# Kernel optimization log

Measured on AMD Instinct MI355X. Metric: run time of the kernel, lower is better.

Reference implementation:

```python
import jax, jax.numpy as jnp
import numpy as np

V_BOOK, V_AUTH, V_LANG, V_TAG = 10001, 5001, 28, 34253
D = 32  # EMBED_DIM
B, C, LH, LW = 4096, 100, 200, 50


def setup_inputs() -> dict:
    key = jax.random.key(0)
    ks = jax.random.split(key, 32)
    it = iter(ks)

    def emb(k, v):
        t = jax.random.normal(k, (v, D), jnp.float32) * 0.05
        return t.at[0].set(0.0)  # padding_idx=0

    def lin(k, i, o):
        k1, k2 = jax.random.split(k)
        lim = 1.0 / np.sqrt(i)
        return (jax.random.uniform(k1, (i, o), jnp.float32, -lim, lim),
                jax.random.uniform(k2, (o,), jnp.float32, -lim, lim))

    hist = jax.random.randint(next(it), (B, LH), 0, V_BOOK)
    wish = jax.random.randint(next(it), (B, LW), 0, V_BOOK)
    cand = jax.random.randint(next(it), (B, C), 0, V_BOOK)
    auth = jax.random.randint(next(it), (B, C), 0, V_AUTH)
    lang = jax.random.randint(next(it), (B, C), 0, V_LANG)
    tags = jax.random.randint(next(it), (B, C, 5), 0, V_TAG)
    dense = jax.random.normal(next(it), (B, C, 3), jnp.float32)

    E_hist = emb(next(it), V_BOOK)
    E_wish = emb(next(it), V_BOOK)
    E_cand = emb(next(it), V_BOOK)
    E_auth = emb(next(it), V_AUTH)
    E_lang = emb(next(it), V_LANG)
    E_tags = emb(next(it), V_TAG)

    Wb0, bb0 = lin(next(it), 3, 32)
    Wb1, bb1 = lin(next(it), 32, D)
    Wt0, bt0 = lin(next(it), 2 * D, 256)
    Wt1, bt1 = lin(next(it), 256, 128)
    Wt2, bt2 = lin(next(it), 128, 64)
    Wt3, bt3 = lin(next(it), 64, 1)

    return dict(hist=hist, wish=wish, cand=cand, auth=auth, lang=lang, tags=tags,
                dense=dense, E_hist=E_hist, E_wish=E_wish, E_cand=E_cand,
                E_auth=E_auth, E_lang=E_lang, E_tags=E_tags,
                Wb0=Wb0, bb0=bb0, Wb1=Wb1, bb1=bb1,
                Wt0=Wt0, bt0=bt0, Wt1=Wt1, bt1=bt1,
                Wt2=Wt2, bt2=bt2, Wt3=Wt3, bt3=bt3)


def reference(hist, wish, cand, auth, lang, tags, dense,
              E_hist, E_wish, E_cand, E_auth, E_lang, E_tags,
              Wb0, bb0, Wb1, bb1, Wt0, bt0, Wt1, bt1, Wt2, bt2, Wt3, bt3):
    # user side: mean-pooled history + wishlist embeddings  [B, D]
    u_vec = E_hist[hist].mean(axis=1) + E_wish[wish].mean(axis=1)
    # item side: candidate + author + language + mean of 5 tag embeddings  [B, C, D]
    e_t = E_tags[tags].sum(axis=2) / 5.0
    i_vec = E_cand[cand] + E_auth[auth] + E_lang[lang] + e_t
    # bottom MLP on dense features  [B, C, D]
    h = jax.nn.relu(jnp.einsum('bcf,fh->bch', dense, Wb0) + bb0)
    d_vec = jnp.einsum('bch,hd->bcd', h, Wb1) + bb1
    i_final = i_vec + d_vec
    # concat broadcast user vec with item vec  [B, C, 2D]
    u_exp = jnp.broadcast_to(u_vec[:, None, :], (u_vec.shape[0], i_final.shape[1], u_vec.shape[1]))
    x = jnp.concatenate([u_exp, i_final], axis=2)
    # top MLP -> scores [B, C]
    x = jax.nn.relu(x @ Wt0 + bt0)
    x = jax.nn.relu(x @ Wt1 + bt1)
    x = jax.nn.relu(x @ Wt2 + bt2)
    scores = (x @ Wt3 + bt3)[..., 0]
    return scores
```

## Files before the change

kernel.cpp:

```cpp
#include <hip/hip_runtime.h>
#include <hip/hip_bf16.h>
#include <stdint.h>

#define NB 4096
#define NC 100
#define NROWS (NB*NC)
#define NTILES (NROWS/64)
#define GRID_F 768
#define LH 200
#define LW 50

typedef short v8s __attribute__((ext_vector_type(8)));
typedef float v4f __attribute__((ext_vector_type(4)));
typedef float v2f __attribute__((ext_vector_type(2)));

__device__ __forceinline__ v4f mfma16(v8s a, v8s b, v4f c) {
  return __builtin_amdgcn_mfma_f32_16x16x32_bf16(a, b, c, 0, 0, 0);
}

__device__ __forceinline__ uint32_t pkbf(float lo, float hi) {
  uint32_t r;
  asm("v_cvt_pk_bf16_f32 %0, %1, %2" : "=v"(r) : "v"(lo), "v"(hi));
  return r;
}

__device__ __forceinline__ uint16_t bf16r(float f) {
  uint32_t u = __builtin_bit_cast(uint32_t, f);
  u = (u + 0x7fffu + ((u >> 16) & 1u)) >> 16;
  return (uint16_t)u;
}

__device__ __forceinline__ float bf2f(short s) {
  return __builtin_bit_cast(float, (uint32_t)((uint16_t)s) << 16);
}

__device__ __forceinline__ int ntli(const int* p) { return __builtin_nontemporal_load(p); }
__device__ __forceinline__ float ntlf(const float* p) { return __builtin_nontemporal_load(p); }

#define WS_FW 524288
#define FRAG_B1 0
#define FRAG_T0 2
#define FRAG_T1 34
#define FRAG_T2 98
#define NFRAGS 114

__global__ void k_prep(const float* __restrict__ Wb1, const float* __restrict__ Wt0,
                       const float* __restrict__ Wt1, const float* __restrict__ Wt2,
                       uint16_t* __restrict__ fb) {
  int f = blockIdx.x;
  int t = threadIdx.x;
  uint16_t res[2];
  #pragma unroll
  for (int e2 = 0; e2 < 2; ++e2) {
    int e = t * 2 + e2;
    int l = e >> 3, i = e & 7;
    int lr = l & 15, lg = l >> 4;
    float v;
    if (f < FRAG_T0) {
      v = Wb1[(lg * 8 + i) * 32 + 2 * lr + f];
    } else if (f < FRAG_T1) {
      int g = f - FRAG_T0;
      int wv = g >> 3, ch = (g >> 2) & 1, ks = (g >> 1) & 1, p = g & 1;
      int n = ch * 128 + wv * 32 + p * 16 + lr;
      int kl = ks * 32 + lg * 8 + i;
      v = Wt0[kl * 256 + n];
    } else if (f < FRAG_T2) {
      int g = f - FRAG_T1;
      int wv = g >> 4, ch = (g >> 3) & 1, ks = (g >> 1) & 3, p = g & 1;
      int n = wv * 32 + p * 16 + lr;
      int kl = ks * 32 + lg * 8 + i;
      int ok = ch * 128 + (kl & ~31) + ((kl & 31) >> 1) + ((kl & 1) << 4);
      v = Wt1[ok * 128 + n];
    } else {
      int g = f - FRAG_T2;
      int wv = g >> 2, ks = g & 3;
      int n = wv * 16 + lr;
      int kl = ks * 32 + lg * 8 + i;
      int ok = (kl & ~31) + ((kl & 31) >> 1) + ((kl & 1) << 4);
      v = Wt2[ok * 64 + n];
    }
    res[e2] = bf16r(v);
  }
  *(uint32_t*)(fb + (size_t)f * 512 + t * 2) = (uint32_t)res[0] | ((uint32_t)res[1] << 16);
}

__global__ void k_user(const int* __restrict__ hist, const int* __restrict__ wish,
                       const float* __restrict__ Eh, const float* __restrict__ Ew,
                       float* __restrict__ uv) {
  int t = threadIdx.x;
  int d = t & 31;
  int r = (blockIdx.x << 3) + (t >> 5);
  const int* hr = hist + r * LH;
  float s = 0.f;
  #pragma unroll 8
  for (int j = 0; j < LH; ++j) s += Eh[ntli(hr + j) * 32 + d];
  float su = s * (1.0f / LH);
  const int* wr = wish + r * LW;
  s = 0.f;
  #pragma unroll 5
  for (int j = 0; j < LW; ++j) s += Ew[ntli(wr + j) * 32 + d];
  uv[r * 32 + d] = su + s * (1.0f / LW);
}

#define SM_CONST 0
#define SM_X     2688
#define SM_ACT3  10880
#define SM_H     10880
#define SM_ACT   19072
#define SM_BYTES 35456

__global__ __launch_bounds__(256, 3)
void k_fused(const int* __restrict__ cand, const int* __restrict__ auth,
             const int* __restrict__ lang, const int* __restrict__ tags,
             const float* __restrict__ dense,
             const float* __restrict__ Ec, const float* __restrict__ Ea,
             const float* __restrict__ El, const float* __restrict__ Et,
             const float* __restrict__ Wb0, const float* __restrict__ bb0,
             const float* __restrict__ bb1, const float* __restrict__ bt0,
             const float* __restrict__ bt1, const float* __restrict__ bt2,
             const float* __restrict__ Wt3, const float* __restrict__ bt3,
             const float* __restrict__ uvec, const uint16_t* __restrict__ fw,
             float* __restrict__ out) {
  extern __shared__ char sm[];
  const char* fwp = (const char*)fw;
  float* cf = (float*)(sm + SM_CONST);
  const int t = threadIdx.x;
  const int l = t & 63, wv = t >> 6;
  const int lr = l & 15, lg = l >> 4;
  const int q = t & 3, rowl = t >> 2;

  cf[32 + t] = bt0[t];
  if (t < 128) cf[288 + t] = bt1[t];
  if (t < 64)  { cf[416 + t] = bt2[t]; cf[608 + t] = Wt3[t]; }
  if (t < 32)  { cf[t] = bb1[t]; cf[480 + t] = bb0[t]; }
  if (t < 96)  cf[512 + t] = Wb0[t];
  const float bt3v = bt3[0];

  for (int tile = blockIdx.x; tile < NTILES; tile += GRID_F) {
    const int r0 = tile << 6;
    __syncthreads();

    {
      int r = r0 + rowl;
      int b = r / 100;
      const float* up = uvec + b * 32 + q * 8;
      int xrb = SM_X + rowl * 128;
      int sw  = (rowl & 7) << 4;
      #pragma unroll
      for (int u2 = 0; u2 < 4; ++u2)
        *(uint32_t*)(sm + xrb + ((q * 16 + u2 * 4) ^ sw)) = pkbf(up[u2 * 2], up[u2 * 2 + 1]);
      float d0 = ntlf(dense + r * 3 + 0), d1 = ntlf(dense + r * 3 + 1), d2 = ntlf(dense + r * 3 + 2);
      const float* bb0l = cf + 480;
      const float* w0a = cf + 512, *w0b = cf + 544, *w0c = cf + 576;
      int hrb = SM_H + rowl * 64;
      int sw3 = (rowl & 3) << 4;
      #pragma unroll
      for (int u2 = 0; u2 < 4; ++u2) {
        int e0 = q * 8 + u2 * 2, e1 = e0 + 1;
        float h0 = fmaxf(bb0l[e0] + d0 * w0a[e0] + d1 * w0b[e0] + d2 * w0c[e0], 0.f);
        float h1 = fmaxf(bb0l[e1] + d0 * w0a[e1] + d1 * w0b[e1] + d2 * w0c[e1], 0.f);
        *(uint32_t*)(sm + hrb + ((q * 16 + u2 * 4) ^ sw3)) = pkbf(h0, h1);
      }
    }
    __syncthreads();

    {
      int hrow = 16 * wv + lr;
      v8s ah  = *(const v8s*)(sm + SM_H + hrow * 64 + ((lg * 16) ^ ((hrow & 3) << 4)));
      v8s wbl = *(const v8s*)(fwp + (size_t)(FRAG_B1 + 0) * 1024 + l * 16);
      v8s wbh = *(const v8s*)(fwp + (size_t)(FRAG_B1 + 1) * 1024 + l * 16);
      float b0v = cf[2 * lr], b1v = cf[2 * lr + 1];
      v4f dv0 = {b0v, b0v, b0v, b0v};
      v4f dv1 = {b1v, b1v, b1v, b1v};
      dv0 = mfma16(ah, wbl, dv0);
      dv1 = mfma16(ah, wbh, dv1);
      #pragma unroll
      for (int j = 0; j < 4; ++j) {
        int mrow = 16 * wv + lg * 4 + j;
        int rr = r0 + mrow;
        int ic = ntli(cand + rr), ia = ntli(auth + rr), il = ntli(lang + rr);
        const int* tp = tags + rr * 5;
        int t0i = ntli(tp), t1i = ntli(tp + 1), t2i = ntli(tp + 2), t3i = ntli(tp + 3), t4i = ntli(tp + 4);
        int co = 2 * lr;
        v2f ec = *(const v2f*)(Ec + ic * 32 + co);
        v2f ea = *(const v2f*)(Ea + ia * 32 + co);
        v2f el = *(const v2f*)(El + il * 32 + co);
        v2f e0 = *(const v2f*)(Et + t0i * 32 + co);
        v2f e1 = *(const v2f*)(Et + t1i * 32 + co);
        v2f e2 = *(const v2f*)(Et + t2i * 32 + co);
        v2f e3 = *(const v2f*)(Et + t3i * 32 + co);
        v2f e4 = *(const v2f*)(Et + t4i * 32 + co);
        float s0 = ec[0] + ea[0] + el[0] + (e0[0] + e1[0] + e2[0] + e3[0] + e4[0]) * 0.2f + dv0[j];
        float s1 = ec[1] + ea[1] + el[1] + (e0[1] + e1[1] + e2[1] + e3[1] + e4[1]) * 0.2f + dv1[j];
        *(uint32_t*)(sm + SM_X + mrow * 128 + ((64 + 4 * lr) ^ ((mrow & 7) << 4))) = pkbf(s0, s1);
      }
    }
    __syncthreads();

    v4f acc2[2][4];
    #pragma unroll
    for (int ch = 0; ch < 2; ++ch) {
      v4f a1[2][4];
      #pragma unroll
      for (int p = 0; p < 2; ++p) {
        float bv = cf[32 + ch * 128 + wv * 32 + p * 16 + lr];
        #pragma unroll
        for (int m = 0; m < 4; ++m) a1[p][m] = (v4f){bv, bv, bv, bv};
      }
      #pragma unroll
      for (int ks = 0; ks < 2; ++ks) {
        v8s xa[4];
        #pragma unroll
        for (int m = 0; m < 4; ++m)
          xa[m] = *(const v8s*)(sm + SM_X + (m * 16 + lr) * 128 + ((ks * 64 + lg * 16) ^ ((lr & 7) << 4)));
        #pragma unroll
        for (int p = 0; p < 2; ++p) {
          v8s wb = *(const v8s*)(fwp + (size_t)(FRAG_T0 + wv * 8 + ch * 4 + ks * 2 + p) * 1024 + l * 16);
          #pragma unroll
          for (int m = 0; m < 4; ++m) a1[p][m] = mfma16(xa[m], wb, a1[p][m]);
        }
      }
      #pragma unroll
      for (int m = 0; m < 4; ++m) {
        #pragma unroll
        for (int j = 0; j < 4; ++j) {
          int row = m * 16 + lg * 4 + j;
          *(uint32_t*)(sm + SM_ACT + row * 256 + ((wv * 64 + 4 * lr) ^ ((row & 7) << 4)))
            = pkbf(fmaxf(a1[0][m][j], 0.f), fmaxf(a1[1][m][j], 0.f));
        }
      }
      __syncthreads();
      if (ch == 0) {
        #pragma unroll
        for (int p = 0; p < 2; ++p) {
          float bv = cf[288 + wv * 32 + p * 16 + lr];
          #pragma unroll
          for (int m = 0; m < 4; ++m) acc2[p][m] = (v4f){bv, bv, bv, bv};
        }
      }
      #pragma unroll
      for (int ks = 0; ks < 4; ++ks) {
        v8s aa[4];
        #pragma unroll
        for (int m = 0; m < 4; ++m)
          aa[m] = *(const v8s*)(sm + SM_ACT + (m * 16 + lr) * 256 + ((ks * 64 + lg * 16) ^ ((lr & 7) << 4)));
        #pragma unroll
        for (int p = 0; p < 2; ++p) {
          v8s wb = *(const v8s*)(fwp + (size_t)(FRAG_T1 + wv * 16 + ch * 8 + ks * 2 + p) * 1024 + l * 16);
          #pragma unroll
          for (int m = 0; m < 4; ++m) acc2[p][m] = mfma16(aa[m], wb, acc2[p][m]);
        }
      }
      __syncthreads();
    }
    #pragma unroll
    for (int m = 0; m < 4; ++m) {
      #pragma unroll
      for (int j = 0; j < 4; ++j) {
        int row = m * 16 + lg * 4 + j;
        *(uint32_t*)(sm + SM_ACT + row * 256 + ((wv * 64 + 4 * lr) ^ ((row & 7) << 4)))
          = pkbf(fmaxf(acc2[0][m][j], 0.f), fmaxf(acc2[1][m][j], 0.f));
      }
    }
    __syncthreads();

    {
      int n2 = wv * 16 + lr;
      float bv = cf[416 + n2];
      v4f a3[4];
      #pragma unroll
      for (int m = 0; m < 4; ++m) a3[m] = (v4f){bv, bv, bv, bv};
      #pragma unroll
      for (int ks = 0; ks < 4; ++ks) {
        v8s wb = *(const v8s*)(fwp + (size_t)(FRAG_T2 + wv * 4 + ks) * 1024 + l * 16);
        #pragma unroll
        for (int m = 0; m < 4; ++m) {
          v8s aa = *(const v8s*)(sm + SM_ACT + (m * 16 + lr) * 256 + ((ks * 64 + lg * 16) ^ ((lr & 7) << 4)));
          a3[m] = mfma16(aa, wb, a3[m]);
        }
      }
      #pragma unroll
      for (int m = 0; m < 4; ++m) {
        #pragma unroll
        for (int j = 0; j < 4; ++j) {
          int row = m * 16 + lg * 4 + j;
          *(uint16_t*)(sm + SM_ACT3 + row * 128 + ((2 * n2) ^ ((row & 7) << 4))) = bf16r(fmaxf(a3[m][j], 0.f));
        }
      }
    }
    __syncthreads();

    {
      float acc = 0.f;
      int arb = SM_ACT3 + rowl * 128;
      int sw  = (rowl & 7) << 4;
      const float* wt3l = cf + 608;
      #pragma unroll
      for (int hf = 0; hf < 2; ++hf) {
        v8s av = *(const v8s*)(sm + arb + ((q * 32 + hf * 16) ^ sw));
        #pragma unroll
        for (int i = 0; i < 8; ++i) acc += bf2f(av[i]) * wt3l[q * 16 + hf * 8 + i];
      }
      acc += __shfl_xor(acc, 1);
      acc += __shfl_xor(acc, 2);
      if (q == 0) __builtin_nontemporal_store(acc + bt3v, out + r0 + rowl);
    }
  }
}

extern "C" void kernel_launch(void* const* d_in, const int* in_sizes, int n_in,
                              void* d_out, int out_size, void* d_ws, size_t ws_size,
                              hipStream_t stream) {
  const int*   hist  = (const int*)d_in[0];
  const int*   wish  = (const int*)d_in[1];
  const int*   cand  = (const int*)d_in[2];
  const int*   auth  = (const int*)d_in[3];
  const int*   lang  = (const int*)d_in[4];
  const int*   tags  = (const int*)d_in[5];
  const float* dense = (const float*)d_in[6];
  const float* Eh    = (const float*)d_in[7];
  const float* Ew    = (const float*)d_in[8];
  const float* Ec    = (const float*)d_in[9];
  const float* Ea    = (const float*)d_in[10];
  const float* El    = (const float*)d_in[11];
  const float* Et    = (const float*)d_in[12];
  const float* Wb0   = (const float*)d_in[13];
  const float* bb0   = (const float*)d_in[14];
  const float* Wb1   = (const float*)d_in[15];
  const float* bb1   = (const float*)d_in[16];
  const float* Wt0   = (const float*)d_in[17];
  const float* bt0   = (const float*)d_in[18];
  const float* Wt1   = (const float*)d_in[19];
  const float* bt1   = (const float*)d_in[20];
  const float* Wt2   = (const float*)d_in[21];
  const float* bt2   = (const float*)d_in[22];
  const float* Wt3   = (const float*)d_in[23];
  const float* bt3   = (const float*)d_in[24];
  char* wsb = (char*)d_ws;
  float* uv = (float*)wsb;
  uint16_t* fw = (uint16_t*)(wsb + WS_FW);
  float* out = (float*)d_out;

  (void)hipFuncSetAttribute((const void*)k_fused,
                            hipFuncAttributeMaxDynamicSharedMemorySize, SM_BYTES);

  k_prep<<<NFRAGS, 256, 0, stream>>>(Wb1, Wt0, Wt1, Wt2, fw);
  k_user<<<NB / 8, 256, 0, stream>>>(hist, wish, Eh, Ew, uv);
  k_fused<<<GRID_F, 256, SM_BYTES, stream>>>(cand, auth, lang, tags, dense,
      Ec, Ea, El, Et, Wb0, bb0, bb1, bt0, bt1, bt2, Wt3, bt3, uv, fw, out);
}
```

Baseline: 299.6 us.

## Convert embedding tables to bf16 and prefetch next tile's indices into LDS

Adds a per-call kernel that converts all embedding tables to bf16 in workspace, so the user pooling and the item gathers read half the bytes. The fused kernel now loads the next tile's indices, dense features and user vector into registers while the current tile computes, staging the indices in shared memory. It also replaces __syncthreads with a barrier that waits only on LDS counters, and uses a normal store for the output. The bf16 path needs a larger workspace and otherwise falls back to the fp32 path. The extra conversion pass reads all tables every call, which may cost more than the smaller gathers save.

```diff
diff --git a/kernel.cpp b/kernel.cpp
--- a/kernel.cpp
+++ b/kernel.cpp
@@ -13,6 +13,7 @@
 typedef short v8s __attribute__((ext_vector_type(8)));
 typedef float v4f __attribute__((ext_vector_type(4)));
 typedef float v2f __attribute__((ext_vector_type(2)));
+typedef uint32_t v4u __attribute__((ext_vector_type(4)));
 
 __device__ __forceinline__ v4f mfma16(v8s a, v8s b, v4f c) {
   return __builtin_amdgcn_mfma_f32_16x16x32_bf16(a, b, c, 0, 0, 0);
@@ -33,16 +34,58 @@
 __device__ __forceinline__ float bf2f(short s) {
   return __builtin_bit_cast(float, (uint32_t)((uint16_t)s) << 16);
 }
+__device__ __forceinline__ float flo(uint32_t u) { return __builtin_bit_cast(float, u << 16); }
+__device__ __forceinline__ float fhi(uint32_t u) { return __builtin_bit_cast(float, u & 0xffff0000u); }
 
 __device__ __forceinline__ int ntli(const int* p) { return __builtin_nontemporal_load(p); }
 __device__ __forceinline__ float ntlf(const float* p) { return __builtin_nontemporal_load(p); }
 
-#define WS_FW 524288
+__device__ __forceinline__ void barx() {
+  asm volatile("s_waitcnt lgkmcnt(0)" ::: "memory");
+  __builtin_amdgcn_s_barrier();
+  asm volatile("" ::: "memory");
+}
+
+#define OFF_UVB 0
+#define OFF_FW  262144
+#define OFF_TB  393216
+#define O_EC 0
+#define O_EA 640064
+#define O_EL 960128
+#define O_ET 961920
+#define O_EH 3154112
+#define O_EW 3794176
+#define TB_SZ 4434240
+#define WS_NEED (OFF_TB + TB_SZ)
+#define OFF_UVF32 0
+#define OFF_FW32  524288
+
 #define FRAG_B1 0
 #define FRAG_T0 2
 #define FRAG_T1 34
 #define FRAG_T2 98
 #define NFRAGS 114
+
+#define CVT_N 2217120
+__global__ void k_cvt(const float* __restrict__ Ec, const float* __restrict__ Ea,
+                      const float* __restrict__ El, const float* __restrict__ Et,
+                      const float* __restrict__ Eh, const float* __restrict__ Ew,
+                      uint16_t* __restrict__ dst) {
+  int e = (blockIdx.x * 256 + threadIdx.x) * 4;
+  if (e >= CVT_N) return;
+  const float* src; int base;
+  if (e < 320032)       { src = Ec; base = 0; }
+  else if (e < 480064)  { src = Ea; base = 320032; }
+  else if (e < 480960)  { src = El; base = 480064; }
+  else if (e < 1577056) { src = Et; base = 480960; }
+  else if (e < 1897088) { src = Eh; base = 1577056; }
+  else                  { src = Ew; base = 1897088; }
+  const float* p = src + (e - base);
+  float4 v = *(const float4*)p;
+  uint32_t a = pkbf(v.x, v.y), b = pkbf(v.z, v.w);
+  uint32_t* d = (uint32_t*)(dst + e);
+  d[0] = a; d[1] = b;
+}
 
 __global__ void k_prep(const float* __restrict__ Wb1, const float* __restrict__ Wt0,
                        const float* __restrict__ Wt1, const float* __restrict__ Wt2,
@@ -84,9 +127,33 @@
   *(uint32_t*)(fb + (size_t)f * 512 + t * 2) = (uint32_t)res[0] | ((uint32_t)res[1] << 16);
 }
 
-__global__ void k_user(const int* __restrict__ hist, const int* __restrict__ wish,
-                       const float* __restrict__ Eh, const float* __restrict__ Ew,
-                       float* __restrict__ uv) {
+__global__ void k_user_bf(const int* __restrict__ hist, const int* __restrict__ wish,
+                          const char* __restrict__ tb, uint32_t* __restrict__ uvb) {
+  int t = threadIdx.x;
+  int d2 = t & 15;
+  int r = blockIdx.x * 16 + (t >> 4);
+  const uint32_t* Eh32 = (const uint32_t*)(tb + O_EH);
+  const uint32_t* Ew32 = (const uint32_t*)(tb + O_EW);
+  const int* hr = hist + r * LH;
+  float sl = 0.f, sh = 0.f;
+  #pragma unroll 8
+  for (int j = 0; j < LH; ++j) {
+    uint32_t g = Eh32[ntli(hr + j) * 16 + d2];
+    sl += flo(g); sh += fhi(g);
+  }
+  const int* wr = wish + r * LW;
+  float wl = 0.f, wh = 0.f;
+  #pragma unroll 5
+  for (int j = 0; j < LW; ++j) {
+    uint32_t g = Ew32[ntli(wr + j) * 16 + d2];
+    wl += flo(g); wh += fhi(g);
+  }
+  uvb[r * 16 + d2] = pkbf(sl * (1.0f/LH) + wl * (1.0f/LW), sh * (1.0f/LH) + wh * (1.0f/LW));
+}
+
+__global__ void k_user_f32(const int* __restrict__ hist, const int* __restrict__ wish,
+                           const float* __restrict__ Eh, const float* __restrict__ Ew,
+                           float* __restrict__ uv) {
   int t = threadIdx.x;
   int d = t & 31;
   int r = (blockIdx.x << 3) + (t >> 5);
@@ -107,20 +174,23 @@
 #define SM_ACT3  10880
 #define SM_H     10880
 #define SM_ACT   19072
-#define SM_BYTES 35456
-
+#define SM_IDX   35456
+#define SM_BYTES 37504
+
+template<int BF>
 __global__ __launch_bounds__(256, 3)
 void k_fused(const int* __restrict__ cand, const int* __restrict__ auth,
              const int* __restrict__ lang, const int* __restrict__ tags,
              const float* __restrict__ dense,
              const float* __restrict__ Ec, const float* __restrict__ Ea,
              const float* __restrict__ El, const float* __restrict__ Et,
+             const char* __restrict__ tb,
              const float* __restrict__ Wb0, const float* __restrict__ bb0,
              const float* __restrict__ bb1, const float* __restrict__ bt0,
              const float* __restrict__ bt1, const float* __restrict__ bt2,
              const float* __restrict__ Wt3, const float* __restrict__ bt3,
-             const float* __restrict__ uvec, const uint16_t* __restrict__ fw,
-             float* __restrict__ out) {
+             const float* __restrict__ uvec, const uint32_t* __restrict__ uvb,
+             const uint16_t* __restrict__ fw, float* __restrict__ out) {
   extern __shared__ char sm[];
   const char* fwp = (const char*)fw;
   float* cf = (float*)(sm + SM_CONST);
@@ -136,20 +206,51 @@
   if (t < 96)  cf[512 + t] = Wb0[t];
   const float bt3v = bt3[0];
 
+  v4u u4;
+  float4 uf0, uf1;
+  float d3x, d3y, d3z;
+  int i2a, i2b;
+
+  auto ld_tile = [&](int tl) {
+    int rr0 = (tl << 6) + rowl;
+    int b = rr0 / 100;
+    if constexpr (BF) {
+      u4 = *(const v4u*)(uvb + b * 16 + q * 4);
+    } else {
+      uf0 = *(const float4*)(uvec + b * 32 + q * 8);
+      uf1 = *(const float4*)(uvec + b * 32 + q * 8 + 4);
+    }
+    d3x = ntlf(dense + rr0 * 3 + 0);
+    d3y = ntlf(dense + rr0 * 3 + 1);
+    d3z = ntlf(dense + rr0 * 3 + 2);
+    int s0 = q * 2;
+    i2a = (s0 == 0) ? ntli(cand + rr0) : (s0 == 2) ? ntli(lang + rr0)
+        : (s0 == 4) ? ntli(tags + rr0 * 5 + 1) : ntli(tags + rr0 * 5 + 3);
+    i2b = (s0 == 0) ? ntli(auth + rr0) : (s0 == 2) ? ntli(tags + rr0 * 5 + 0)
+        : (s0 == 4) ? ntli(tags + rr0 * 5 + 2) : ntli(tags + rr0 * 5 + 4);
+  };
+
+  ld_tile(blockIdx.x);
+
   for (int tile = blockIdx.x; tile < NTILES; tile += GRID_F) {
     const int r0 = tile << 6;
-    __syncthreads();
+    barx();
 
     {
-      int r = r0 + rowl;
-      int b = r / 100;
-      const float* up = uvec + b * 32 + q * 8;
       int xrb = SM_X + rowl * 128;
       int sw  = (rowl & 7) << 4;
-      #pragma unroll
-      for (int u2 = 0; u2 < 4; ++u2)
-        *(uint32_t*)(sm + xrb + ((q * 16 + u2 * 4) ^ sw)) = pkbf(up[u2 * 2], up[u2 * 2 + 1]);
-      float d0 = ntlf(dense + r * 3 + 0), d1 = ntlf(dense + r * 3 + 1), d2 = ntlf(dense + r * 3 + 2);
+      if constexpr (BF) {
+        #pragma unroll
+        for (int k2 = 0; k2 < 4; ++k2)
+          *(uint32_t*)(sm + xrb + ((q * 16 + k2 * 4) ^ sw)) = u4[k2];
+      } else {
+        float uu[8] = {uf0.x, uf0.y, uf0.z, uf0.w, uf1.x, uf1.y, uf1.z, uf1.w};
+        #pragma unroll
+        for (int k2 = 0; k2 < 4; ++k2)
+          *(uint32_t*)(sm + xrb + ((q * 16 + k2 * 4) ^ sw)) = pkbf(uu[2*k2], uu[2*k2+1]);
+      }
+      *(int*)(sm + SM_IDX + rowl * 32 + q * 8)     = i2a;
+      *(int*)(sm + SM_IDX + rowl * 32 + q * 8 + 4) = i2b;
       const float* bb0l = cf + 480;
       const float* w0a = cf + 512, *w0b = cf + 544, *w0c = cf + 576;
       int hrb = SM_H + rowl * 64;
@@ -157,12 +258,14 @@
       #pragma unroll
       for (int u2 = 0; u2 < 4; ++u2) {
         int e0 = q * 8 + u2 * 2, e1 = e0 + 1;
-        float h0 = fmaxf(bb0l[e0] + d0 * w0a[e0] + d1 * w0b[e0] + d2 * w0c[e0], 0.f);
-        float h1 = fmaxf(bb0l[e1] + d0 * w0a[e1] + d1 * w0b[e1] + d2 * w0c[e1], 0.f);
+        float h0 = fmaxf(bb0l[e0] + d3x * w0a[e0] + d3y * w0b[e0] + d3z * w0c[e0], 0.f);
+        float h1 = fmaxf(bb0l[e1] + d3x * w0a[e1] + d3y * w0b[e1] + d3z * w0c[e1], 0.f);
         *(uint32_t*)(sm + hrb + ((q * 16 + u2 * 4) ^ sw3)) = pkbf(h0, h1);
       }
     }
-    __syncthreads();
+    barx();
+
+    if (tile + GRID_F < NTILES) ld_tile(tile + GRID_F);
 
     {
       int hrow = 16 * wv + lr;
@@ -177,25 +280,40 @@
       #pragma unroll
       for (int j = 0; j < 4; ++j) {
         int mrow = 16 * wv + lg * 4 + j;
-        int rr = r0 + mrow;
-        int ic = ntli(cand + rr), ia = ntli(auth + rr), il = ntli(lang + rr);
-        const int* tp = tags + rr * 5;
-        int t0i = ntli(tp), t1i = ntli(tp + 1), t2i = ntli(tp + 2), t3i = ntli(tp + 3), t4i = ntli(tp + 4);
-        int co = 2 * lr;
-        v2f ec = *(const v2f*)(Ec + ic * 32 + co);
-        v2f ea = *(const v2f*)(Ea + ia * 32 + co);
-        v2f el = *(const v2f*)(El + il * 32 + co);
-        v2f e0 = *(const v2f*)(Et + t0i * 32 + co);
-        v2f e1 = *(const v2f*)(Et + t1i * 32 + co);
-        v2f e2 = *(const v2f*)(Et + t2i * 32 + co);
-        v2f e3 = *(const v2f*)(Et + t3i * 32 + co);
-        v2f e4 = *(const v2f*)(Et + t4i * 32 + co);
-        float s0 = ec[0] + ea[0] + el[0] + (e0[0] + e1[0] + e2[0] + e3[0] + e4[0]) * 0.2f + dv0[j];
-        float s1 = ec[1] + ea[1] + el[1] + (e0[1] + e1[1] + e2[1] + e3[1] + e4[1]) * 0.2f + dv1[j];
+        const int* ip = (const int*)(sm + SM_IDX + mrow * 32);
+        int ic = ip[0], ia = ip[1], il = ip[2];
+        int t0i = ip[3], t1i = ip[4], t2i = ip[5], t3i = ip[6], t4i = ip[7];
+        float s0, s1;
+        if constexpr (BF) {
+          uint32_t gc = *(const uint32_t*)(tb + O_EC + (size_t)ic * 64 + lr * 4);
+          uint32_t ga = *(const uint32_t*)(tb + O_EA + (size_t)ia * 64 + lr * 4);
+          uint32_t gl = *(const uint32_t*)(tb + O_EL + (size_t)il * 64 + lr * 4);
+          uint32_t g0 = *(const uint32_t*)(tb + O_ET + (size_t)t0i * 64 + lr * 4);
+          uint32_t g1 = *(const uint32_t*)(tb + O_ET + (size_t)t1i * 64 + lr * 4);
+          uint32_t g2 = *(const uint32_t*)(tb + O_ET + (size_t)t2i * 64 + lr * 4);
+          uint32_t g3 = *(const uint32_t*)(tb + O_ET + (size_t)t3i * 64 + lr * 4);
+          uint32_t g4 = *(const uint32_t*)(tb + O_ET + (size_t)t4i * 64 + lr * 4);
+          s0 = flo(gc) + flo(ga) + flo(gl)
+             + (flo(g0) + flo(g1) + flo(g2) + flo(g3) + flo(g4)) * 0.2f + dv0[j];
+          s1 = fhi(gc) + fhi(ga) + fhi(gl)
+             + (fhi(g0) + fhi(g1) + fhi(g2) + fhi(g3) + fhi(g4)) * 0.2f + dv1[j];
+        } else {
+          int co = 2 * lr;
+          v2f ec = *(const v2f*)(Ec + ic * 32 + co);
+          v2f ea = *(const v2f*)(Ea + ia * 32 + co);
+          v2f el = *(const v2f*)(El + il * 32 + co);
+          v2f e0 = *(const v2f*)(Et + t0i * 32 + co);
+          v2f e1 = *(const v2f*)(Et + t1i * 32 + co);
+          v2f e2 = *(const v2f*)(Et + t2i * 32 + co);
+          v2f e3 = *(const v2f*)(Et + t3i * 32 + co);
+          v2f e4 = *(const v2f*)(Et + t4i * 32 + co);
+          s0 = ec[0] + ea[0] + el[0] + (e0[0]+e1[0]+e2[0]+e3[0]+e4[0]) * 0.2f + dv0[j];
+          s1 = ec[1] + ea[1] + el[1] + (e0[1]+e1[1]+e2[1]+e3[1]+e4[1]) * 0.2f + dv1[j];
+        }
         *(uint32_t*)(sm + SM_X + mrow * 128 + ((64 + 4 * lr) ^ ((mrow & 7) << 4))) = pkbf(s0, s1);
       }
     }
-    __syncthreads();
+    barx();
 
     v4f acc2[2][4];
     #pragma unroll
@@ -229,7 +347,7 @@
             = pkbf(fmaxf(a1[0][m][j], 0.f), fmaxf(a1[1][m][j], 0.f));
         }
       }
-      __syncthreads();
+      barx();
       if (ch == 0) {
         #pragma unroll
         for (int p = 0; p < 2; ++p) {
@@ -251,7 +369,7 @@
           for (int m = 0; m < 4; ++m) acc2[p][m] = mfma16(aa[m], wb, acc2[p][m]);
         }
       }
-      __syncthreads();
+      barx();
     }
     #pragma unroll
     for (int m = 0; m < 4; ++m) {
@@ -262,7 +380,7 @@
           = pkbf(fmaxf(acc2[0][m][j], 0.f), fmaxf(acc2[1][m][j], 0.f));
       }
     }
-    __syncthreads();
+    barx();
 
     {
       int n2 = wv * 16 + lr;
@@ -288,7 +406,7 @@
         }
       }
     }
-    __syncthreads();
+    barx();
 
     {
       float acc = 0.f;
@@ -303,7 +421,7 @@
       }
       acc += __shfl_xor(acc, 1);
       acc += __shfl_xor(acc, 2);
-      if (q == 0) __builtin_nontemporal_store(acc + bt3v, out + r0 + rowl);
+      if (q == 0) out[r0 + rowl] = acc + bt3v;
     }
   }
 }
@@ -337,15 +455,31 @@
   const float* Wt3   = (const float*)d_in[23];
   const float* bt3   = (const float*)d_in[24];
   char* wsb = (char*)d_ws;
-  float* uv = (float*)wsb;
-  uint16_t* fw = (uint16_t*)(wsb + WS_FW);
   float* out = (float*)d_out;
 
-  (void)hipFuncSetAttribute((const void*)k_fused,
-                            hipFuncAttributeMaxDynamicSharedMemorySize, SM_BYTES);
-
-  k_prep<<<NFRAGS, 256, 0, stream>>>(Wb1, Wt0, Wt1, Wt2, fw);
-  k_user<<<NB / 8, 256, 0, stream>>>(hist, wish, Eh, Ew, uv);
-  k_fused<<<GRID_F, 256, SM_BYTES, stream>>>(cand, auth, lang, tags, dense,
-      Ec, Ea, El, Et, Wb0, bb0, bb1, bt0, bt1, bt2, Wt3, bt3, uv, fw, out);
-}
+  if (ws_size >= (size_t)WS_NEED) {
+    uint32_t* uvb = (uint32_t*)(wsb + OFF_UVB);
+    uint16_t* fw  = (uint16_t*)(wsb + OFF_FW);
+    char*     tb  = wsb + OFF_TB;
+    auto kf = k_fused<1>;
+    (void)hipFuncSetAttribute((const void*)kf,
+                              hipFuncAttributeMaxDynamicSharedMemorySize, SM_BYTES);
+    k_cvt<<<(CVT_N / 4 + 255) / 256, 256, 0, stream>>>(Ec, Ea, El, Et, Eh, Ew, (uint16_t*)tb);
+    k_prep<<<NFRAGS, 256, 0, stream>>>(Wb1, Wt0, Wt1, Wt2, fw);
+    k_user_bf<<<NB / 16, 256, 0, stream>>>(hist, wish, tb, uvb);
+    kf<<<GRID_F, 256, SM_BYTES, stream>>>(cand, auth, lang, tags, dense,
+        Ec, Ea, El, Et, tb, Wb0, bb0, bb1, bt0, bt1, bt2, Wt3, bt3,
+        (const float*)nullptr, uvb, fw, out);
+  } else {
+    float*    uv = (float*)(wsb + OFF_UVF32);
+    uint16_t* fw = (uint16_t*)(wsb + OFF_FW32);
+    auto kf = k_fused<0>;
+    (void)hipFuncSetAttribute((const void*)kf,
+                              hipFuncAttributeMaxDynamicSharedMemorySize, SM_BYTES);
+    k_prep<<<NFRAGS, 256, 0, stream>>>(Wb1, Wt0, Wt1, Wt2, fw);
+    k_user_f32<<<NB / 8, 256, 0, stream>>>(hist, wish, Eh, Ew, uv);
+    kf<<<GRID_F, 256, SM_BYTES, stream>>>(cand, auth, lang, tags, dense,
+        Ec, Ea, El, Et, (const char*)nullptr, Wb0, bb0, bb1, bt0, bt1, bt2, Wt3, bt3,
+        uv, (const uint32_t*)nullptr, fw, out);
+  }
+}
```

New measurement: 290.2 us. 1.03x faster.

## Software-pipeline embedding gathers across tiles and restructure MLP stage barriers

Applied to the files above, without the earlier changes.

Index loads for the tile two steps ahead and embedding gathers for the next tile are now issued during the final MLP stage, staged through a shared-memory index buffer, so gather latency overlaps compute. The layer-1 activations are stored in full width, which removes the per-chunk barriers. The layer-3 mapping is changed so the final dot product reduces in registers via shuffles, dropping one LDS round-trip. The user vector is precomputed in bf16 with vectorized loads, and plain __syncthreads is replaced by a custom lgkmcnt wait plus barrier. The cost is higher register pressure from holding 32 prefetched v2f values and more LDS (about 49KB), which risks occupancy at 3 blocks per SM.

```diff
diff --git a/kernel.cpp b/kernel.cpp
--- a/kernel.cpp
+++ b/kernel.cpp
@@ -13,6 +13,7 @@
 typedef short v8s __attribute__((ext_vector_type(8)));
 typedef float v4f __attribute__((ext_vector_type(4)));
 typedef float v2f __attribute__((ext_vector_type(2)));
+typedef uint32_t v4u __attribute__((ext_vector_type(4)));
 
 __device__ __forceinline__ v4f mfma16(v8s a, v8s b, v4f c) {
   return __builtin_amdgcn_mfma_f32_16x16x32_bf16(a, b, c, 0, 0, 0);
@@ -30,14 +31,18 @@
   return (uint16_t)u;
 }
 
-__device__ __forceinline__ float bf2f(short s) {
-  return __builtin_bit_cast(float, (uint32_t)((uint16_t)s) << 16);
-}
-
 __device__ __forceinline__ int ntli(const int* p) { return __builtin_nontemporal_load(p); }
 __device__ __forceinline__ float ntlf(const float* p) { return __builtin_nontemporal_load(p); }
 
-#define WS_FW 524288
+__device__ __forceinline__ void barx() {
+  asm volatile("s_waitcnt lgkmcnt(0)" ::: "memory");
+  __builtin_amdgcn_s_barrier();
+  asm volatile("" ::: "memory");
+}
+
+#define OFF_UVB 0
+#define OFF_FW  262144
+
 #define FRAG_B1 0
 #define FRAG_T0 2
 #define FRAG_T1 34
@@ -73,8 +78,8 @@
       v = Wt1[ok * 128 + n];
     } else {
       int g = f - FRAG_T2;
-      int wv = g >> 2, ks = g & 3;
-      int n = wv * 16 + lr;
+      int gc = g >> 2, ks = g & 3;
+      int n = gc * 16 + lr;
       int kl = ks * 32 + lg * 8 + i;
       int ok = (kl & ~31) + ((kl & 31) >> 1) + ((kl & 1) << 4);
       v = Wt2[ok * 64 + n];
@@ -84,30 +89,36 @@
   *(uint32_t*)(fb + (size_t)f * 512 + t * 2) = (uint32_t)res[0] | ((uint32_t)res[1] << 16);
 }
 
-__global__ void k_user(const int* __restrict__ hist, const int* __restrict__ wish,
-                       const float* __restrict__ Eh, const float* __restrict__ Ew,
-                       float* __restrict__ uv) {
+__global__ void k_user_bf(const int* __restrict__ hist, const int* __restrict__ wish,
+                          const float* __restrict__ Eh, const float* __restrict__ Ew,
+                          uint32_t* __restrict__ uvb) {
   int t = threadIdx.x;
-  int d = t & 31;
-  int r = (blockIdx.x << 3) + (t >> 5);
+  int d2 = t & 15;
+  int r = blockIdx.x * 16 + (t >> 4);
   const int* hr = hist + r * LH;
-  float s = 0.f;
+  float sl = 0.f, sh = 0.f;
   #pragma unroll 8
-  for (int j = 0; j < LH; ++j) s += Eh[ntli(hr + j) * 32 + d];
-  float su = s * (1.0f / LH);
+  for (int j = 0; j < LH; ++j) {
+    v2f e = *(const v2f*)(Eh + ntli(hr + j) * 32 + 2 * d2);
+    sl += e[0]; sh += e[1];
+  }
   const int* wr = wish + r * LW;
-  s = 0.f;
+  float wl = 0.f, wh = 0.f;
   #pragma unroll 5
-  for (int j = 0; j < LW; ++j) s += Ew[ntli(wr + j) * 32 + d];
-  uv[r * 32 + d] = su + s * (1.0f / LW);
+  for (int j = 0; j < LW; ++j) {
+    v2f e = *(const v2f*)(Ew + ntli(wr + j) * 32 + 2 * d2);
+    wl += e[0]; wh += e[1];
+  }
+  uvb[r * 16 + d2] = pkbf(sl * (1.0f/LH) + wl * (1.0f/LW), sh * (1.0f/LH) + wh * (1.0f/LW));
 }
 
 #define SM_CONST 0
 #define SM_X     2688
-#define SM_ACT3  10880
 #define SM_H     10880
-#define SM_ACT   19072
-#define SM_BYTES 35456
+#define SM_ACT1  14976
+#define SM_ACT2  14976
+#define SM_IDX   47744
+#define SM_BYTES 49792
 
 __global__ __launch_bounds__(256, 3)
 void k_fused(const int* __restrict__ cand, const int* __restrict__ auth,
@@ -119,7 +130,7 @@
              const float* __restrict__ bb1, const float* __restrict__ bt0,
              const float* __restrict__ bt1, const float* __restrict__ bt2,
              const float* __restrict__ Wt3, const float* __restrict__ bt3,
-             const float* __restrict__ uvec, const uint16_t* __restrict__ fw,
+             const uint32_t* __restrict__ uvb, const uint16_t* __restrict__ fw,
              float* __restrict__ out) {
   extern __shared__ char sm[];
   const char* fwp = (const char*)fw;
@@ -136,20 +147,68 @@
   if (t < 96)  cf[512 + t] = Wb0[t];
   const float bt3v = bt3[0];
 
-  for (int tile = blockIdx.x; tile < NTILES; tile += GRID_F) {
+  v8s wbl = *(const v8s*)(fwp + (size_t)(FRAG_B1 + 0) * 1024 + l * 16);
+  v8s wbh = *(const v8s*)(fwp + (size_t)(FRAG_B1 + 1) * 1024 + l * 16);
+
+  v4u u4;
+  float d3x, d3y, d3z;
+  int i2a, i2b;
+  v2f gc[4], ga[4], gl[4], gt0[4], gt1[4], gt2[4], gt3[4], gt4[4];
+
+  auto ld_uv = [&](int tl) {
+    int rr0 = (tl << 6) + rowl;
+    int b = rr0 / 100;
+    u4 = *(const v4u*)(uvb + b * 16 + q * 4);
+    d3x = ntlf(dense + rr0 * 3 + 0);
+    d3y = ntlf(dense + rr0 * 3 + 1);
+    d3z = ntlf(dense + rr0 * 3 + 2);
+  };
+  auto ld_idx = [&](int tl) {
+    int rr0 = (tl << 6) + rowl;
+    int s0 = q * 2;
+    i2a = (s0 == 0) ? ntli(cand + rr0) : (s0 == 2) ? ntli(lang + rr0)
+        : (s0 == 4) ? ntli(tags + rr0 * 5 + 1) : ntli(tags + rr0 * 5 + 3);
+    i2b = (s0 == 0) ? ntli(auth + rr0) : (s0 == 2) ? ntli(tags + rr0 * 5 + 0)
+        : (s0 == 4) ? ntli(tags + rr0 * 5 + 2) : ntli(tags + rr0 * 5 + 4);
+  };
+  auto issue_gathers = [&]() {
+    #pragma unroll
+    for (int j = 0; j < 4; ++j) {
+      int mrow = 16 * wv + lg * 4 + j;
+      const int* ip = (const int*)(sm + SM_IDX + mrow * 32);
+      int ic = ip[0], ia = ip[1], il = ip[2];
+      int x0 = ip[3], x1 = ip[4], x2 = ip[5], x3 = ip[6], x4 = ip[7];
+      gc[j]  = *(const v2f*)(Ec + ic * 32 + 2 * lr);
+      ga[j]  = *(const v2f*)(Ea + ia * 32 + 2 * lr);
+      gl[j]  = *(const v2f*)(El + il * 32 + 2 * lr);
+      gt0[j] = *(const v2f*)(Et + x0 * 32 + 2 * lr);
+      gt1[j] = *(const v2f*)(Et + x1 * 32 + 2 * lr);
+      gt2[j] = *(const v2f*)(Et + x2 * 32 + 2 * lr);
+      gt3[j] = *(const v2f*)(Et + x3 * 32 + 2 * lr);
+      gt4[j] = *(const v2f*)(Et + x4 * 32 + 2 * lr);
+    }
+  };
+
+  const int tile0 = blockIdx.x;
+  ld_idx(tile0);
+  *(int*)(sm + SM_IDX + rowl * 32 + q * 8)     = i2a;
+  *(int*)(sm + SM_IDX + rowl * 32 + q * 8 + 4) = i2b;
+  barx();
+  issue_gathers();
+  ld_uv(tile0);
+  { int n1 = tile0 + GRID_F; if (n1 > NTILES - 1) n1 = NTILES - 1; ld_idx(n1); }
+
+  for (int tile = tile0; tile < NTILES; tile += GRID_F) {
     const int r0 = tile << 6;
-    __syncthreads();
 
     {
-      int r = r0 + rowl;
-      int b = r / 100;
-      const float* up = uvec + b * 32 + q * 8;
       int xrb = SM_X + rowl * 128;
       int sw  = (rowl & 7) << 4;
       #pragma unroll
-      for (int u2 = 0; u2 < 4; ++u2)
-        *(uint32_t*)(sm + xrb + ((q * 16 + u2 * 4) ^ sw)) = pkbf(up[u2 * 2], up[u2 * 2 + 1]);
-      float d0 = ntlf(dense + r * 3 + 0), d1 = ntlf(dense + r * 3 + 1), d2 = ntlf(dense + r * 3 + 2);
+      for (int k2 = 0; k2 < 4; ++k2)
+        *(uint32_t*)(sm + xrb + ((q * 16 + k2 * 4) ^ sw)) = u4[k2];
+      *(int*)(sm + SM_IDX + rowl * 32 + q * 8)     = i2a;
+      *(int*)(sm + SM_IDX + rowl * 32 + q * 8 + 4) = i2b;
       const float* bb0l = cf + 480;
       const float* w0a = cf + 512, *w0b = cf + 544, *w0c = cf + 576;
       int hrb = SM_H + rowl * 64;
@@ -157,18 +216,16 @@
       #pragma unroll
       for (int u2 = 0; u2 < 4; ++u2) {
         int e0 = q * 8 + u2 * 2, e1 = e0 + 1;
-        float h0 = fmaxf(bb0l[e0] + d0 * w0a[e0] + d1 * w0b[e0] + d2 * w0c[e0], 0.f);
-        float h1 = fmaxf(bb0l[e1] + d0 * w0a[e1] + d1 * w0b[e1] + d2 * w0c[e1], 0.f);
+        float h0 = fmaxf(bb0l[e0] + d3x * w0a[e0] + d3y * w0b[e0] + d3z * w0c[e0], 0.f);
+        float h1 = fmaxf(bb0l[e1] + d3x * w0a[e1] + d3y * w0b[e1] + d3z * w0c[e1], 0.f);
         *(uint32_t*)(sm + hrb + ((q * 16 + u2 * 4) ^ sw3)) = pkbf(h0, h1);
       }
     }
-    __syncthreads();
+    barx();
 
     {
       int hrow = 16 * wv + lr;
-      v8s ah  = *(const v8s*)(sm + SM_H + hrow * 64 + ((lg * 16) ^ ((hrow & 3) << 4)));
-      v8s wbl = *(const v8s*)(fwp + (size_t)(FRAG_B1 + 0) * 1024 + l * 16);
-      v8s wbh = *(const v8s*)(fwp + (size_t)(FRAG_B1 + 1) * 1024 + l * 16);
+      v8s ah = *(const v8s*)(sm + SM_H + hrow * 64 + ((lg * 16) ^ ((hrow & 3) << 4)));
       float b0v = cf[2 * lr], b1v = cf[2 * lr + 1];
       v4f dv0 = {b0v, b0v, b0v, b0v};
       v4f dv1 = {b1v, b1v, b1v, b1v};
@@ -177,27 +234,15 @@
       #pragma unroll
       for (int j = 0; j < 4; ++j) {
         int mrow = 16 * wv + lg * 4 + j;
-        int rr = r0 + mrow;
-        int ic = ntli(cand + rr), ia = ntli(auth + rr), il = ntli(lang + rr);
-        const int* tp = tags + rr * 5;
-        int t0i = ntli(tp), t1i = ntli(tp + 1), t2i = ntli(tp + 2), t3i = ntli(tp + 3), t4i = ntli(tp + 4);
-        int co = 2 * lr;
-        v2f ec = *(const v2f*)(Ec + ic * 32 + co);
-        v2f ea = *(const v2f*)(Ea + ia * 32 + co);
-        v2f el = *(const v2f*)(El + il * 32 + co);
-        v2f e0 = *(const v2f*)(Et + t0i * 32 + co);
-        v2f e1 = *(const v2f*)(Et + t1i * 32 + co);
-        v2f e2 = *(const v2f*)(Et + t2i * 32 + co);
-        v2f e3 = *(const v2f*)(Et + t3i * 32 + co);
-        v2f e4 = *(const v2f*)(Et + t4i * 32 + co);
-        float s0 = ec[0] + ea[0] + el[0] + (e0[0] + e1[0] + e2[0] + e3[0] + e4[0]) * 0.2f + dv0[j];
-        float s1 = ec[1] + ea[1] + el[1] + (e0[1] + e1[1] + e2[1] + e3[1] + e4[1]) * 0.2f + dv1[j];
+        float s0 = gc[j][0] + ga[j][0] + gl[j][0]
+                 + (gt0[j][0] + gt1[j][0] + gt2[j][0] + gt3[j][0] + gt4[j][0]) * 0.2f + dv0[j];
+        float s1 = gc[j][1] + ga[j][1] + gl[j][1]
+                 + (gt0[j][1] + gt1[j][1] + gt2[j][1] + gt3[j][1] + gt4[j][1]) * 0.2f + dv1[j];
         *(uint32_t*)(sm + SM_X + mrow * 128 + ((64 + 4 * lr) ^ ((mrow & 7) << 4))) = pkbf(s0, s1);
       }
     }
-    __syncthreads();
-
-    v4f acc2[2][4];
+    barx();
+
     #pragma unroll
     for (int ch = 0; ch < 2; ++ch) {
       v4f a1[2][4];
@@ -209,15 +254,13 @@
       }
       #pragma unroll
       for (int ks = 0; ks < 2; ++ks) {
-        v8s xa[4];
-        #pragma unroll
-        for (int m = 0; m < 4; ++m)
-          xa[m] = *(const v8s*)(sm + SM_X + (m * 16 + lr) * 128 + ((ks * 64 + lg * 16) ^ ((lr & 7) << 4)));
-        #pragma unroll
-        for (int p = 0; p < 2; ++p) {
-          v8s wb = *(const v8s*)(fwp + (size_t)(FRAG_T0 + wv * 8 + ch * 4 + ks * 2 + p) * 1024 + l * 16);
-          #pragma unroll
-          for (int m = 0; m < 4; ++m) a1[p][m] = mfma16(xa[m], wb, a1[p][m]);
+        v8s f0 = *(const v8s*)(fwp + (size_t)(FRAG_T0 + wv * 8 + ch * 4 + ks * 2 + 0) * 1024 + l * 16);
+        v8s f1 = *(const v8s*)(fwp + (size_t)(FRAG_T0 + wv * 8 + ch * 4 + ks * 2 + 1) * 1024 + l * 16);
+        #pragma unroll
+        for (int m = 0; m < 4; ++m) {
+          v8s xa = *(const v8s*)(sm + SM_X + (m * 16 + lr) * 128 + ((ks * 64 + lg * 16) ^ ((lr & 7) << 4)));
+          a1[0][m] = mfma16(xa, f0, a1[0][m]);
+          a1[1][m] = mfma16(xa, f1, a1[1][m]);
         }
       }
       #pragma unroll
@@ -225,86 +268,87 @@
         #pragma unroll
         for (int j = 0; j < 4; ++j) {
           int row = m * 16 + lg * 4 + j;
-          *(uint32_t*)(sm + SM_ACT + row * 256 + ((wv * 64 + 4 * lr) ^ ((row & 7) << 4)))
+          *(uint32_t*)(sm + SM_ACT1 + row * 512 + ((ch * 256 + wv * 64 + 4 * lr) ^ ((row & 7) << 4)))
             = pkbf(fmaxf(a1[0][m][j], 0.f), fmaxf(a1[1][m][j], 0.f));
         }
       }
-      __syncthreads();
-      if (ch == 0) {
-        #pragma unroll
-        for (int p = 0; p < 2; ++p) {
-          float bv = cf[288 + wv * 32 + p * 16 + lr];
-          #pragma unroll
-          for (int m = 0; m < 4; ++m) acc2[p][m] = (v4f){bv, bv, bv, bv};
+    }
+    barx();
+
+    v4f acc2[2][4];
+    #pragma unroll
+    for (int p = 0; p < 2; ++p) {
+      float bv = cf[288 + wv * 32 + p * 16 + lr];
+      #pragma unroll
+      for (int m = 0; m < 4; ++m) acc2[p][m] = (v4f){bv, bv, bv, bv};
+    }
+    #pragma unroll
+    for (int ch = 0; ch < 2; ++ch) {
+      #pragma unroll
+      for (int ks = 0; ks < 4; ++ks) {
+        v8s f0 = *(const v8s*)(fwp + (size_t)(FRAG_T1 + wv * 16 + ch * 8 + ks * 2 + 0) * 1024 + l * 16);
+        v8s f1 = *(const v8s*)(fwp + (size_t)(FRAG_T1 + wv * 16 + ch * 8 + ks * 2 + 1) * 1024 + l * 16);
+        #pragma unroll
+        for (int m = 0; m < 4; ++m) {
+          v8s aa = *(const v8s*)(sm + SM_ACT1 + (m * 16 + lr) * 512 + ((ch * 256 + ks * 64 + lg * 16) ^ ((lr & 7) << 4)));
+          acc2[0][m] = mfma16(aa, f0, acc2[0][m]);
+          acc2[1][m] = mfma16(aa, f1, acc2[1][m]);
         }
       }
-      #pragma unroll
-      for (int ks = 0; ks < 4; ++ks) {
-        v8s aa[4];
-        #pragma unroll
-        for (int m = 0; m < 4; ++m)
-          aa[m] = *(const v8s*)(sm + SM_ACT + (m * 16 + lr) * 256 + ((ks * 64 + lg * 16) ^ ((lr & 7) << 4)));
-        #pragma unroll
-        for (int p = 0; p < 2; ++p) {
-          v8s wb = *(const v8s*)(fwp + (size_t)(FRAG_T1 + wv * 16 + ch * 8 + ks * 2 + p) * 1024 + l * 16);
-          #pragma unroll
-          for (int m = 0; m < 4; ++m) acc2[p][m] = mfma16(aa[m], wb, acc2[p][m]);
-        }
-      }
-      __syncthreads();
-    }
+    }
+    barx();
+
     #pragma unroll
     for (int m = 0; m < 4; ++m) {
       #pragma unroll
       for (int j = 0; j < 4; ++j) {
         int row = m * 16 + lg * 4 + j;
-        *(uint32_t*)(sm + SM_ACT + row * 256 + ((wv * 64 + 4 * lr) ^ ((row & 7) << 4)))
+        *(uint32_t*)(sm + SM_ACT2 + row * 256 + ((wv * 64 + 4 * lr) ^ ((row & 7) << 4)))
           = pkbf(fmaxf(acc2[0][m][j], 0.f), fmaxf(acc2[1][m][j], 0.f));
       }
     }
-    __syncthreads();
+    barx();
 
     {
-      int n2 = wv * 16 + lr;
-      float bv = cf[416 + n2];
-      v4f a3[4];
-      #pragma unroll
-      for (int m = 0; m < 4; ++m) a3[m] = (v4f){bv, bv, bv, bv};
+      int arow = 16 * wv + lr;
+      float bv0 = cf[416 + lr],      bv1 = cf[416 + 16 + lr];
+      float bv2 = cf[416 + 32 + lr], bv3 = cf[416 + 48 + lr];
+      v4f a3[4] = {{bv0, bv0, bv0, bv0}, {bv1, bv1, bv1, bv1},
+                   {bv2, bv2, bv2, bv2}, {bv3, bv3, bv3, bv3}};
       #pragma unroll
       for (int ks = 0; ks < 4; ++ks) {
-        v8s wb = *(const v8s*)(fwp + (size_t)(FRAG_T2 + wv * 4 + ks) * 1024 + l * 16);
-        #pragma unroll
-        for (int m = 0; m < 4; ++m) {
-          v8s aa = *(const v8s*)(sm + SM_ACT + (m * 16 + lr) * 256 + ((ks * 64 + lg * 16) ^ ((lr & 7) << 4)));
-          a3[m] = mfma16(aa, wb, a3[m]);
+        v8s aa = *(const v8s*)(sm + SM_ACT2 + arow * 256 + ((ks * 64 + lg * 16) ^ ((arow & 7) << 4)));
+        #pragma unroll
+        for (int g = 0; g < 4; ++g) {
+          v8s fg = *(const v8s*)(fwp + (size_t)(FRAG_T2 + g * 4 + ks) * 1024 + l * 16);
+          a3[g] = mfma16(aa, fg, a3[g]);
         }
       }
-      #pragma unroll
-      for (int m = 0; m < 4; ++m) {
-        #pragma unroll
-        for (int j = 0; j < 4; ++j) {
-          int row = m * 16 + lg * 4 + j;
-          *(uint16_t*)(sm + SM_ACT3 + row * 128 + ((2 * n2) ^ ((row & 7) << 4))) = bf16r(fmaxf(a3[m][j], 0.f));
-        }
-      }
-    }
-    __syncthreads();
-
-    {
-      float acc = 0.f;
-      int arb = SM_ACT3 + rowl * 128;
-      int sw  = (rowl & 7) << 4;
-      const float* wt3l = cf + 608;
-      #pragma unroll
-      for (int hf = 0; hf < 2; ++hf) {
-        v8s av = *(const v8s*)(sm + arb + ((q * 32 + hf * 16) ^ sw));
-        #pragma unroll
-        for (int i = 0; i < 8; ++i) acc += bf2f(av[i]) * wt3l[q * 16 + hf * 8 + i];
-      }
-      acc += __shfl_xor(acc, 1);
-      acc += __shfl_xor(acc, 2);
-      if (q == 0) __builtin_nontemporal_store(acc + bt3v, out + r0 + rowl);
-    }
+
+      int n1 = tile + GRID_F;     if (n1 > NTILES - 1) n1 = NTILES - 1;
+      int n2 = tile + 2 * GRID_F; if (n2 > NTILES - 1) n2 = NTILES - 1;
+      ld_uv(n1);
+      ld_idx(n2);
+      issue_gathers();
+
+      float wr0 = cf[608 + lr],      wr1 = cf[608 + 16 + lr];
+      float wr2 = cf[608 + 32 + lr], wr3 = cf[608 + 48 + lr];
+      float o[4];
+      #pragma unroll
+      for (int j = 0; j < 4; ++j) {
+        o[j] = fmaxf(a3[0][j], 0.f) * wr0 + fmaxf(a3[1][j], 0.f) * wr1
+             + fmaxf(a3[2][j], 0.f) * wr2 + fmaxf(a3[3][j], 0.f) * wr3;
+        o[j] += __shfl_xor(o[j], 1);
+        o[j] += __shfl_xor(o[j], 2);
+        o[j] += __shfl_xor(o[j], 4);
+        o[j] += __shfl_xor(o[j], 8);
+      }
+      if (lr == 0) {
+        float4 ov = {o[0] + bt3v, o[1] + bt3v, o[2] + bt3v, o[3] + bt3v};
+        *(float4*)(out + r0 + wv * 16 + lg * 4) = ov;
+      }
+    }
+    barx();
   }
 }
 
@@ -337,15 +381,16 @@
   const float* Wt3   = (const float*)d_in[23];
   const float* bt3   = (const float*)d_in[24];
   char* wsb = (char*)d_ws;
-  float* uv = (float*)wsb;
-  uint16_t* fw = (uint16_t*)(wsb + WS_FW);
   float* out = (float*)d_out;
+
+  uint32_t* uvb = (uint32_t*)(wsb + OFF_UVB);
+  uint16_t* fw  = (uint16_t*)(wsb + OFF_FW);
 
   (void)hipFuncSetAttribute((const void*)k_fused,
                             hipFuncAttributeMaxDynamicSharedMemorySize, SM_BYTES);
 
   k_prep<<<NFRAGS, 256, 0, stream>>>(Wb1, Wt0, Wt1, Wt2, fw);
-  k_user<<<NB / 8, 256, 0, stream>>>(hist, wish, Eh, Ew, uv);
+  k_user_bf<<<NB / 16, 256, 0, stream>>>(hist, wish, Eh, Ew, uvb);
   k_fused<<<GRID_F, 256, SM_BYTES, stream>>>(cand, auth, lang, tags, dense,
-      Ec, Ea, El, Et, Wb0, bb0, bb1, bt0, bt1, bt2, Wt3, bt3, uv, fw, out);
-}
+      Ec, Ea, El, Et, Wb0, bb0, bb1, bt0, bt1, bt2, Wt3, bt3, uvb, fw, out);
+}
```

New measurement: 325.4 us. 1.09x slower.
